# Kernel tuning notes

Measured on AMD Instinct MI355X. Metric: run time of the kernel, lower is better.

Reference implementation:

```python
import jax, jax.numpy as jnp
import numpy as np

N_POI, EMBED, N_EDGES, N_LAYERS, N_HEADS = 50000, 128, 800000, 2, 4
B, L = 512, 64  # sessions, session length (equal-length sections)


def setup_inputs() -> dict:
    key = jax.random.key(0)
    ks = jax.random.split(key, 12)
    d = EMBED
    return {
        "poi_embeds": jax.random.normal(ks[0], (N_POI, d), jnp.float32),
        "dist_edges": jax.random.randint(ks[1], (2, N_EDGES), 0, N_POI),
        "dist_vec": jax.random.uniform(ks[2], (N_EDGES,), jnp.float32),
        "data_poi": jax.random.randint(ks[3], (B,), 0, N_POI),
        "data_x": jax.random.randint(ks[4], (B * L,), 0, N_POI),
        "lin_w": jax.random.normal(ks[5], (N_LAYERS, d, d), jnp.float32) / np.sqrt(d),
        "lin_b": jnp.zeros((N_LAYERS, d), jnp.float32),
        "in_proj_w": jax.random.normal(ks[6], (3 * d, d), jnp.float32) / np.sqrt(d),
        "in_proj_b": jnp.zeros((3 * d,), jnp.float32),
        "out_proj_w": jax.random.normal(ks[7], (d, d), jnp.float32) / np.sqrt(d),
        "out_proj_b": jnp.zeros((d,), jnp.float32),
    }


def reference(poi_embeds, dist_edges, dist_vec, data_poi, data_x,
              lin_w, lin_b, in_proj_w, in_proj_b, out_proj_w, out_proj_b):
    n_poi, d = poi_embeds.shape
    # --- edge augmentation done in GeoGraph.__init__: reversed edges + self loops ---
    loop = jnp.arange(n_poi)
    edges = jnp.concatenate([dist_edges, dist_edges[::-1], jnp.stack([loop, loop])], axis=1)
    dvec = jnp.concatenate([dist_vec, dist_vec, jnp.zeros((n_poi,), dist_vec.dtype)])
    src, dst = edges[0], edges[1]
    # degree of source nodes (torch_geometric.utils.degree on nodes1)
    deg = jnp.zeros((n_poi,), poi_embeds.dtype).at[src].add(1.0)
    w = jax.lax.rsqrt(deg[src] * deg[dst]) * jnp.exp(-dvec ** 2)  # [E]

    enc = poi_embeds
    for i in range(lin_w.shape[0]):
        h = enc @ lin_w[i].T + lin_b[i]                              # [N, d]
        msg = w[:, None] * h[dst]                                    # [E, d] gather
        agg = jax.ops.segment_sum(msg, src, num_segments=n_poi)      # [N, d] scatter
        agg = jnp.where(agg >= 0, agg, 0.01 * agg)                   # leaky_relu(0.01)
        enc = agg / jnp.maximum(jnp.linalg.norm(agg, axis=-1, keepdims=True), 1e-12)

    tar_embed = enc[data_poi]                                        # [B, d]
    seq = enc[data_x].reshape(B, L, d)                               # padded sessions

    # --- nn.MultiheadAttention (batch_first) ---
    hd = d // N_HEADS
    qkv = seq @ in_proj_w.T + in_proj_b                              # [B, L, 3d]
    q, k, v = jnp.split(qkv, 3, axis=-1)
    heads = lambda t: t.reshape(B, L, N_HEADS, hd).transpose(0, 2, 1, 3)
    q, k, v = heads(q), heads(k), heads(v)
    scores = jnp.einsum('bhqd,bhkd->bhqk', q, k) / np.sqrt(hd)
    attn = jax.nn.softmax(scores, axis=-1)
    o = jnp.einsum('bhqk,bhkd->bhqd', attn, v).transpose(0, 2, 1, 3).reshape(B, L, d)
    o = o @ out_proj_w.T + out_proj_b

    aggr_feat = o.mean(axis=1)                                       # mean over padded length
    return aggr_feat, tar_embed
```

## Files before the change

kernel.cpp:

```cpp
#include <hip/hip_runtime.h>
#include <hip/hip_fp16.h>
#include <type_traits>

#define NPOI 50000
#define EMB 128
#define NEDGE 800000
#define EAUG (2 * NEDGE + NPOI)
#define BATCH 512
#define SEQL 64
#define NHEADS 4
#define HDIM 32
#define SCAN_BLOCKS ((NPOI + 255) / 256)
#define NB SCAN_BLOCKS
#define P1_BLOCKS ((NEDGE + 2047) / 2048)
#define SLAB_CAP 10240
#define BUCKET_CAP 10240

typedef _Float16 half8 __attribute__((ext_vector_type(8)));
typedef _Float16 half4 __attribute__((ext_vector_type(4)));
typedef _Float16 half2t __attribute__((ext_vector_type(2)));
typedef float f32x4 __attribute__((ext_vector_type(4)));
typedef unsigned long long u64;

union HBits { _Float16 h; unsigned short u; };


#define N4_POI (NPOI * 128 / 4)
#define N4_LIN (2 * 128 * 128 / 4)
#define N4_INW (384 * 128 / 4)

__global__ void cvt_all_kernel(const float* __restrict__ poi, const float* __restrict__ linw,
                               const float* __restrict__ inw,
                               _Float16* __restrict__ poi_h, _Float16* __restrict__ linw_h,
                               _Float16* __restrict__ inw_h) {
    int i = blockIdx.x * blockDim.x + threadIdx.x;
    const float* src; _Float16* dst; int j = i;
    if (i < N4_POI) { src = poi; dst = poi_h; }
    else if (i < N4_POI + N4_LIN) { j = i - N4_POI; src = linw; dst = linw_h; }
    else if (i < N4_POI + N4_LIN + N4_INW) { j = i - N4_POI - N4_LIN; src = inw; dst = inw_h; }
    else return;
    float4 v = ((const float4*)src)[j];
    half4 h = { (_Float16)v.x, (_Float16)v.y, (_Float16)v.z, (_Float16)v.w };
    ((half4*)dst)[j] = h;
}

__global__ void init_bcur_kernel(int* __restrict__ bcur) {
    int t = blockIdx.x * blockDim.x + threadIdx.x;
    if (t < NB) bcur[t] = t * SLAB_CAP;
}


__global__ __launch_bounds__(256) void partition_kernel(
    const int* __restrict__ e0, const int* __restrict__ e1,
    const float* __restrict__ dv, int* __restrict__ bcur,
    u64* __restrict__ staging)
{
    __shared__ u64 stg[4096];
    __shared__ int lh[NB], lbase[NB], gb[NB];
    __shared__ int sc[256];
    const int t = threadIdx.x;
    const int blockBase = blockIdx.x * 2048;
    for (int j = t; j < NB; j += 256) lh[j] = 0;
    __syncthreads();

    u64 vals[16];
    unsigned br[16];
#pragma unroll
    for (int i = 0; i < 8; ++i) {
        br[2 * i] = 0xFFFFFFFFu;
        br[2 * i + 1] = 0xFFFFFFFFu;
        int g = blockBase + i * 256 + t;
        if (g < NEDGE) {
            int s = e0[g], d = e1[g];
            unsigned db = __float_as_uint(dv[g]);
            vals[2 * i]     = ((u64)s << 48) | ((u64)d << 32) | db;
            vals[2 * i + 1] = ((u64)d << 48) | ((u64)s << 32) | db;
            int bs = s >> 8, bd = d >> 8;
            int rs = atomicAdd(&lh[bs], 1);
            int rd_ = atomicAdd(&lh[bd], 1);
            br[2 * i]     = ((unsigned)bs << 16) | (unsigned)rs;
            br[2 * i + 1] = ((unsigned)bd << 16) | (unsigned)rd_;
        }
    }
    __syncthreads();
    sc[t] = (t < NB) ? lh[t] : 0;
    __syncthreads();
    for (int o = 1; o < 256; o <<= 1) {
        int u = (t >= o) ? sc[t - o] : 0;
        __syncthreads();
        sc[t] += u;
        __syncthreads();
    }
    if (t < NB) {
        lbase[t] = sc[t] - lh[t];
        gb[t] = (lh[t] > 0) ? atomicAdd(&bcur[t], lh[t]) : 0;
    }
    __syncthreads();
#pragma unroll
    for (int i = 0; i < 16; ++i) {
        if (br[i] != 0xFFFFFFFFu) {
            int b = br[i] >> 16, r = br[i] & 0xFFFF;
            stg[lbase[b] + r] = vals[i];
        }
    }
    __syncthreads();
    const int total = sc[255];
    for (int j = t; j < total; j += 256) {
        u64 v = stg[j];
        int b = (int)(v >> 56);
        staging[(size_t)gb[b] + (unsigned)(j - lbase[b])] = v;
    }
}


__global__ __launch_bounds__(256) void hist_kernel(const u64* __restrict__ staging,
                                                   const int* __restrict__ bcur,
                                                   int* __restrict__ counts,
                                                   int* __restrict__ bsum) {
    __shared__ int cnt[256];
    __shared__ int red[256];
    const int b = blockIdx.x, t = threadIdx.x;
    cnt[t] = 0;
    __syncthreads();
    const int base = b * SLAB_CAP;
    const int n = bcur[b] - base;
    for (int j = t; j < n; j += 256)
        atomicAdd(&cnt[(int)(staging[base + j] >> 48) & 255], 1);
    __syncthreads();
    int node = b * 256 + t;
    int rowsz = 0;
    if (node < NPOI) {
        counts[node] = cnt[t];
        rowsz = cnt[t] + 1;
    }
    red[t] = rowsz;
    __syncthreads();
    for (int o = 128; o > 0; o >>= 1) {
        if (t < o) red[t] += red[t + o];
        __syncthreads();
    }
    if (t == 0) bsum[b] = red[0];
}

__global__ __launch_bounds__(256) void scan_chunk_kernel(const int* __restrict__ counts,
                                                         const int* __restrict__ bsum,
                                                         int* __restrict__ offs,
                                                         float* __restrict__ rd) {
    __shared__ int shb[256];
    __shared__ int sh[256];
    __shared__ int base_sh;
    int b = blockIdx.x, t = threadIdx.x;
    shb[t] = (t < SCAN_BLOCKS) ? bsum[t] : 0;
    __syncthreads();
    int partial = 0;
    for (int j = t; j < b; j += 256) partial += shb[j];
    sh[t] = partial;
    __syncthreads();
    for (int o = 128; o > 0; o >>= 1) {
        if (t < o) sh[t] += sh[t + o];
        __syncthreads();
    }
    if (t == 0) base_sh = sh[0];
    __syncthreads();
    int bbase = base_sh;
    __syncthreads();
    int i = b * 256 + t;
    int v = (i < NPOI) ? (counts[i] + 1) : 0;
    sh[t] = v;
    __syncthreads();
    for (int o = 1; o < 256; o <<= 1) {
        int u = (t >= o) ? sh[t - o] : 0;
        __syncthreads();
        sh[t] += u;
        __syncthreads();
    }
    int excl = sh[t] - v + bbase;
    if (i < NPOI) {
        offs[i] = excl;
        rd[i] = rsqrtf((float)v);
        if (i == NPOI - 1) offs[NPOI] = excl + v;
    }
}


__global__ __launch_bounds__(256) void csr_sort_kernel(
    const u64* __restrict__ staging, const int* __restrict__ bcur,
    const int* __restrict__ offs, const float* __restrict__ rd,
    unsigned* __restrict__ ew)
{
    const int k = blockIdx.x;
    const int node0 = k * 256;
    const int node1 = (node0 + 256 < NPOI) ? node0 + 256 : NPOI;
    __shared__ unsigned outb[BUCKET_CAP];
    __shared__ int cnt[256], base2[256];
    __shared__ float rdl[256];
    const int t = threadIdx.x;
    const int node = node0 + t;
    cnt[t] = 0;
    rdl[t] = (node < NPOI) ? rd[node] : 0.f;
    __syncthreads();
    const int sb = k * SLAB_CAP;
    const int n = bcur[k] - sb;
    for (int j = t; j < n; j += 256)
        atomicAdd(&cnt[(int)(staging[sb + j] >> 48) & 255], 1);
    __syncthreads();
    int rowsz = (node < NPOI) ? cnt[t] + 1 : 0;
    base2[t] = rowsz;
    __syncthreads();
    for (int o = 1; o < 256; o <<= 1) {
        int u = (t >= o) ? base2[t - o] : 0;
        __syncthreads();
        base2[t] += u;
        __syncthreads();
    }
    int myexc = base2[t] - rowsz;
    __syncthreads();
    base2[t] = myexc;
    cnt[t] = 0;
    __syncthreads();
    for (int j = t; j < n; j += 256) {
        u64 e = staging[sb + j];
        int sl = (int)(e >> 48) & 255;
        int d = (int)(e >> 32) & 0xFFFF;
        float dist = __uint_as_float((unsigned)e);
        float w = rdl[sl] * rd[d] * expf(-dist * dist);
        HBits cv; cv.h = (_Float16)w;
        int r = atomicAdd(&cnt[sl], 1);
        outb[base2[sl] + r] = ((unsigned)d << 16) | cv.u;
    }
    __syncthreads();
    if (node < NPOI) {
        float w = rdl[t] * rdl[t];
        HBits cv; cv.h = (_Float16)w;
        outb[base2[t] + cnt[t]] = ((unsigned)node << 16) | cv.u;
    }
    __syncthreads();
    const int beg = offs[node0];
    const int ntot = offs[node1] - beg;
    for (int j = t; j < ntot; j += 256) ew[beg + j] = outb[j];
}


template <typename OutT>
__global__ __launch_bounds__(256) void gemm_mfma_f16(
    const _Float16* __restrict__ A, const int* __restrict__ gidx,
    const _Float16* __restrict__ B, const float* __restrict__ bias,
    OutT* __restrict__ C, int M, int N)
{
    __shared__ _Float16 Asl[64][136];
    __shared__ _Float16 Bsl[64][136];
    const int tid = threadIdx.x;
    const int n0 = blockIdx.x * 64;
    const int m0 = blockIdx.y * 64;

#pragma unroll
    for (int i = 0; i < 4; ++i) {
        int u = i * 256 + tid;
        int r = u >> 4;
        int c = u & 15;
        int row = m0 + r;
        int ar = (row < M) ? (gidx ? gidx[row] : row) : 0;
        *(float4*)&Asl[r][c * 8] = *(const float4*)(A + (size_t)ar * 128 + c * 8);
        *(float4*)&Bsl[r][c * 8] = *(const float4*)(B + (size_t)(n0 + r) * 128 + c * 8);
    }
    __syncthreads();

    const int wave = tid >> 6;
    const int lane = tid & 63;
    const int l15 = lane & 15;
    const int quad = lane >> 4;

    f32x4 acc[4];
#pragma unroll
    for (int mt = 0; mt < 4; ++mt) acc[mt] = (f32x4){0.f, 0.f, 0.f, 0.f};

#pragma unroll
    for (int ks = 0; ks < 4; ++ks) {
        half8 bfrag = *(const half8*)&Bsl[wave * 16 + l15][quad * 8 + ks * 32];
#pragma unroll
        for (int mt = 0; mt < 4; ++mt) {
            half8 afrag = *(const half8*)&Asl[mt * 16 + l15][quad * 8 + ks * 32];
            acc[mt] = __builtin_amdgcn_mfma_f32_16x16x32_f16(afrag, bfrag, acc[mt], 0, 0, 0);
        }
    }

    int col = n0 + wave * 16 + l15;
    float bv = bias[col];
#pragma unroll
    for (int mt = 0; mt < 4; ++mt) {
#pragma unroll
        for (int r = 0; r < 4; ++r) {
            int m = m0 + mt * 16 + quad * 4 + r;
            if (m < M) {
                float v = acc[mt][r] + bv;
                if constexpr (std::is_same<OutT, _Float16>::value)
                    C[(size_t)m * N + col] = (_Float16)v;
                else
                    C[(size_t)m * N + col] = v;
            }
        }
    }
}


__global__ __launch_bounds__(64) void aggregate_kernel(
    const _Float16* __restrict__ h, const int* __restrict__ offs,
    const unsigned* __restrict__ ew, float* __restrict__ enc_out,
    _Float16* __restrict__ enc_h)
{
    const int row = blockIdx.x;
    const int lane = threadIdx.x;
    const int beg = offs[row];
    const int end = offs[row + 1];
    float ax = 0.f, ay = 0.f;
#pragma unroll 4
    for (int e = beg; e < end; ++e) {
        unsigned p = ew[e];
        HBits cv; cv.u = (unsigned short)(p & 0xffffu);
        float w = (float)cv.h;
        int d = p >> 16;
        half2t hv = *(const half2t*)(h + (size_t)d * 128 + lane * 2);
        ax += w * (float)hv[0];
        ay += w * (float)hv[1];
    }
    ax = ax >= 0.f ? ax : 0.01f * ax;
    ay = ay >= 0.f ? ay : 0.01f * ay;
    float ss = ax * ax + ay * ay;
#pragma unroll
    for (int o = 32; o > 0; o >>= 1) ss += __shfl_xor(ss, o);
    float inv = 1.f / fmaxf(sqrtf(ss), 1e-12f);
    float ex = ax * inv, ey = ay * inv;
    *(float2*)(enc_out + (size_t)row * 128 + lane * 2) = make_float2(ex, ey);
    half2t hv = { (_Float16)ex, (_Float16)ey };
    *(half2t*)(enc_h + (size_t)row * 128 + lane * 2) = hv;
}


__global__ __launch_bounds__(256) void attn_mfma_kernel(
    const _Float16* __restrict__ qkv, const float* __restrict__ outw,
    const float* __restrict__ outb, float* __restrict__ out)
{
    const int b = blockIdx.x;
    const int wave = threadIdx.x >> 6;
    const int lane = threadIdx.x & 63;
    const int l15 = lane & 15;
    const int quad = lane >> 4;
    __shared__ _Float16 pP[NHEADS][64][72];
    __shared__ _Float16 vT[NHEADS][32][72];
    __shared__ float ob[128];
    const _Float16* base = qkv + (size_t)b * SEQL * 384;

    {
        const _Float16* vrow = base + (size_t)lane * 384 + 256 + wave * 32;
        half8 v0 = *(const half8*)(vrow);
        half8 v1 = *(const half8*)(vrow + 8);
        half8 v2 = *(const half8*)(vrow + 16);
        half8 v3 = *(const half8*)(vrow + 24);
#pragma unroll
        for (int j = 0; j < 8; ++j) {
            vT[wave][j][lane]      = v0[j];
            vT[wave][j + 8][lane]  = v1[j];
            vT[wave][j + 16][lane] = v2[j];
            vT[wave][j + 24][lane] = v3[j];
        }
    }

    half8 qf[4], kf[4];
#pragma unroll
    for (int t = 0; t < 4; ++t) {
        qf[t] = *(const half8*)(base + (size_t)(t * 16 + l15) * 384 + wave * 32 + quad * 8);
        kf[t] = *(const half8*)(base + (size_t)(t * 16 + l15) * 384 + 128 + wave * 32 + quad * 8);
    }

    f32x4 S[4][4];
#pragma unroll
    for (int lt = 0; lt < 4; ++lt)
#pragma unroll
        for (int mt = 0; mt < 4; ++mt) S[lt][mt] = (f32x4){0.f, 0.f, 0.f, 0.f};
#pragma unroll
    for (int lt = 0; lt < 4; ++lt)
#pragma unroll
        for (int mt = 0; mt < 4; ++mt)
            S[lt][mt] = __builtin_amdgcn_mfma_f32_16x16x32_f16(qf[lt], kf[mt], S[lt][mt], 0, 0, 0);

    const float scale = 0.17677669529663687f;
#pragma unroll
    for (int lt = 0; lt < 4; ++lt) {
#pragma unroll
        for (int r = 0; r < 4; ++r) {
            float m0 = -1e30f;
#pragma unroll
            for (int mt = 0; mt < 4; ++mt) {
                S[lt][mt][r] *= scale;
                m0 = fmaxf(m0, S[lt][mt][r]);
            }
#pragma unroll
            for (int o = 1; o < 16; o <<= 1) m0 = fmaxf(m0, __shfl_xor(m0, o));
            float s0 = 0.f;
#pragma unroll
            for (int mt = 0; mt < 4; ++mt) {
                float p = __expf(S[lt][mt][r] - m0);
                S[lt][mt][r] = p;
                s0 += p;
            }
#pragma unroll
            for (int o = 1; o < 16; o <<= 1) s0 += __shfl_xor(s0, o);
            float inv = 1.f / s0;
#pragma unroll
            for (int mt = 0; mt < 4; ++mt)
                pP[wave][lt * 16 + quad * 4 + r][mt * 16 + l15] = (_Float16)(S[lt][mt][r] * inv);
        }
    }
    __syncthreads();

    f32x4 O[4][2];
#pragma unroll
    for (int lt = 0; lt < 4; ++lt)
#pragma unroll
        for (int jt = 0; jt < 2; ++jt) O[lt][jt] = (f32x4){0.f, 0.f, 0.f, 0.f};
#pragma unroll
    for (int kh = 0; kh < 2; ++kh) {
        half8 vf[2];
#pragma unroll
        for (int jt = 0; jt < 2; ++jt)
            vf[jt] = *(const half8*)&vT[wave][jt * 16 + l15][kh * 32 + quad * 8];
#pragma unroll
        for (int lt = 0; lt < 4; ++lt) {
            half8 pf = *(const half8*)&pP[wave][lt * 16 + l15][kh * 32 + quad * 8];
#pragma unroll
            for (int jt = 0; jt < 2; ++jt)
                O[lt][jt] = __builtin_amdgcn_mfma_f32_16x16x32_f16(pf, vf[jt], O[lt][jt], 0, 0, 0);
        }
    }

#pragma unroll
    for (int jt = 0; jt < 2; ++jt) {
        float part = 0.f;
#pragma unroll
        for (int lt = 0; lt < 4; ++lt)
#pragma unroll
            for (int r = 0; r < 4; ++r) part += O[lt][jt][r];
        part += __shfl_xor(part, 16);
        part += __shfl_xor(part, 32);
        if (quad == 0) ob[wave * 32 + jt * 16 + l15] = part * (1.f / 64.f);
    }
    __syncthreads();

    int t = threadIdx.x;
    if (t < 128) {
        float val = outb[t];
        const float* wrow = outw + (size_t)t * 128;
#pragma unroll 8
        for (int k4 = 0; k4 < 32; ++k4) {
            float4 wv = *(const float4*)(wrow + k4 * 4);
            val += wv.x * ob[k4 * 4] + wv.y * ob[k4 * 4 + 1]
                 + wv.z * ob[k4 * 4 + 2] + wv.w * ob[k4 * 4 + 3];
        }
        out[(size_t)b * 128 + t] = val;
    }
}


__global__ void tar_kernel(const float* __restrict__ enc, const int* __restrict__ data_poi,
                           float* __restrict__ out)
{
    int i = blockIdx.x * blockDim.x + threadIdx.x;
    if (i >= BATCH * 128) return;
    int r = i >> 7, c = i & 127;
    out[i] = enc[(size_t)data_poi[r] * 128 + c];
}


extern "C" void kernel_launch(void* const* d_in, const int* in_sizes, int n_in,
                              void* d_out, int out_size, void* d_ws, size_t ws_size,
                              hipStream_t stream)
{
    const float* poi      = (const float*)d_in[0];
    const int*   edges    = (const int*)d_in[1];
    const float* dvec     = (const float*)d_in[2];
    const int*   data_poi = (const int*)d_in[3];
    const int*   data_x   = (const int*)d_in[4];
    const float* lin_w    = (const float*)d_in[5];
    const float* lin_b    = (const float*)d_in[6];
    const float* inw      = (const float*)d_in[7];
    const float* inb      = (const float*)d_in[8];
    const float* outw     = (const float*)d_in[9];
    const float* outb     = (const float*)d_in[10];
    const int* e0 = edges;
    const int* e1 = edges + NEDGE;

    char* ws = (char*)d_ws;
    size_t off = 0;
    auto alloc = [&](size_t bytes) -> void* {
        void* p = ws + off;
        off = (off + bytes + 255) & ~(size_t)255;
        return p;
    };
    int*      counts = (int*)     alloc(NPOI * 4);
    int*      offs   = (int*)     alloc((NPOI + 1) * 4);
    int*      bsum   = (int*)     alloc(SCAN_BLOCKS * 4);
    int*      bcur   = (int*)     alloc(NB * 4);
    float*    rd     = (float*)   alloc(NPOI * 4);
    unsigned* ew     = (unsigned*)alloc((size_t)EAUG * 4);
    float*    enc    = (float*)   alloc((size_t)NPOI * 128 * 4);
    _Float16* enc_h  = (_Float16*)alloc((size_t)NPOI * 128 * 2);
    _Float16* linw_h = (_Float16*)alloc((size_t)2 * 128 * 128 * 2);
    _Float16* inw_h  = (_Float16*)alloc((size_t)384 * 128 * 2);
    char*     big    = (char*)    alloc(50ull * 1024 * 1024);
    _Float16* poi_h   = (_Float16*)big;
    u64*      staging = (u64*)(big + 16ull * 1024 * 1024);
    _Float16* hbuf    = (_Float16*)(big + 33ull * 1024 * 1024);
    _Float16* qkv_h   = (_Float16*)big;

    cvt_all_kernel<<<(N4_POI + N4_LIN + N4_INW + 255) / 256, 256, 0, stream>>>(
        poi, lin_w, inw, poi_h, linw_h, inw_h);

    init_bcur_kernel<<<1, 256, 0, stream>>>(bcur);
    partition_kernel<<<P1_BLOCKS, 256, 0, stream>>>(e0, e1, dvec, bcur, staging);
    hist_kernel<<<NB, 256, 0, stream>>>(staging, bcur, counts, bsum);
    scan_chunk_kernel<<<SCAN_BLOCKS, 256, 0, stream>>>(counts, bsum, offs, rd);
    csr_sort_kernel<<<NB, 256, 0, stream>>>(staging, bcur, offs, rd, ew);

    gemm_mfma_f16<_Float16><<<dim3(2, (NPOI + 63) / 64), 256, 0, stream>>>(
        poi_h, nullptr, linw_h, lin_b, hbuf, NPOI, 128);
    aggregate_kernel<<<NPOI, 64, 0, stream>>>(hbuf, offs, ew, enc, enc_h);
    gemm_mfma_f16<_Float16><<<dim3(2, (NPOI + 63) / 64), 256, 0, stream>>>(
        enc_h, nullptr, linw_h + 128 * 128, lin_b + 128, hbuf, NPOI, 128);
    aggregate_kernel<<<NPOI, 64, 0, stream>>>(hbuf, offs, ew, enc, enc_h);

    gemm_mfma_f16<_Float16><<<dim3(6, BATCH * SEQL / 64), 256, 0, stream>>>(
        enc_h, data_x, inw_h, inb, qkv_h, BATCH * SEQL, 384);
    attn_mfma_kernel<<<BATCH, 256, 0, stream>>>(qkv_h, outw, outb, (float*)d_out);

    tar_kernel<<<(BATCH * 128 + 255) / 256, 256, 0, stream>>>(
        enc, data_poi, (float*)d_out + BATCH * 128);
}
```

Measured before the change: 307.2 us.

## Fuse small setup kernels, stage GEMM epilogue through LDS, merge target gather into attention

```diff
diff --git a/kernel.cpp b/kernel.cpp
--- a/kernel.cpp
+++ b/kernel.cpp
@@ -1,6 +1,5 @@
 #include <hip/hip_runtime.h>
 #include <hip/hip_fp16.h>
-#include <type_traits>
 
 #define NPOI 50000
 #define EMB 128
@@ -10,8 +9,7 @@
 #define SEQL 64
 #define NHEADS 4
 #define HDIM 32
-#define SCAN_BLOCKS ((NPOI + 255) / 256)
-#define NB SCAN_BLOCKS
+#define NB 196
 #define P1_BLOCKS ((NEDGE + 2047) / 2048)
 #define SLAB_CAP 10240
 #define BUCKET_CAP 10240
@@ -28,25 +26,22 @@
 #define N4_POI (NPOI * 128 / 4)
 #define N4_LIN (2 * 128 * 128 / 4)
 #define N4_INW (384 * 128 / 4)
+#define CVT_TOT (N4_POI + N4_LIN + N4_INW + NB)
 
 __global__ void cvt_all_kernel(const float* __restrict__ poi, const float* __restrict__ linw,
                                const float* __restrict__ inw,
                                _Float16* __restrict__ poi_h, _Float16* __restrict__ linw_h,
-                               _Float16* __restrict__ inw_h) {
+                               _Float16* __restrict__ inw_h, int* __restrict__ bcur) {
     int i = blockIdx.x * blockDim.x + threadIdx.x;
     const float* src; _Float16* dst; int j = i;
     if (i < N4_POI) { src = poi; dst = poi_h; }
     else if (i < N4_POI + N4_LIN) { j = i - N4_POI; src = linw; dst = linw_h; }
     else if (i < N4_POI + N4_LIN + N4_INW) { j = i - N4_POI - N4_LIN; src = inw; dst = inw_h; }
+    else if (i < CVT_TOT) { int b = i - (N4_POI + N4_LIN + N4_INW); bcur[b] = b * SLAB_CAP; return; }
     else return;
     float4 v = ((const float4*)src)[j];
     half4 h = { (_Float16)v.x, (_Float16)v.y, (_Float16)v.z, (_Float16)v.w };
     ((half4*)dst)[j] = h;
-}
-
-__global__ void init_bcur_kernel(int* __restrict__ bcur) {
-    int t = blockIdx.x * blockDim.x + threadIdx.x;
-    if (t < NB) bcur[t] = t * SLAB_CAP;
 }
 
 
@@ -115,7 +110,7 @@
 
 __global__ __launch_bounds__(256) void hist_kernel(const u64* __restrict__ staging,
                                                    const int* __restrict__ bcur,
-                                                   int* __restrict__ counts,
+                                                   float* __restrict__ rd,
                                                    int* __restrict__ bsum) {
     __shared__ int cnt[256];
     __shared__ int red[256];
@@ -130,8 +125,8 @@
     int node = b * 256 + t;
     int rowsz = 0;
     if (node < NPOI) {
-        counts[node] = cnt[t];
         rowsz = cnt[t] + 1;
+        rd[node] = rsqrtf((float)rowsz);
     }
     red[t] = rowsz;
     __syncthreads();
@@ -142,62 +137,35 @@
     if (t == 0) bsum[b] = red[0];
 }
 
-__global__ __launch_bounds__(256) void scan_chunk_kernel(const int* __restrict__ counts,
-                                                         const int* __restrict__ bsum,
-                                                         int* __restrict__ offs,
-                                                         float* __restrict__ rd) {
-    __shared__ int shb[256];
-    __shared__ int sh[256];
-    __shared__ int base_sh;
-    int b = blockIdx.x, t = threadIdx.x;
-    shb[t] = (t < SCAN_BLOCKS) ? bsum[t] : 0;
-    __syncthreads();
-    int partial = 0;
-    for (int j = t; j < b; j += 256) partial += shb[j];
-    sh[t] = partial;
-    __syncthreads();
-    for (int o = 128; o > 0; o >>= 1) {
-        if (t < o) sh[t] += sh[t + o];
-        __syncthreads();
-    }
-    if (t == 0) base_sh = sh[0];
-    __syncthreads();
-    int bbase = base_sh;
-    __syncthreads();
-    int i = b * 256 + t;
-    int v = (i < NPOI) ? (counts[i] + 1) : 0;
-    sh[t] = v;
-    __syncthreads();
-    for (int o = 1; o < 256; o <<= 1) {
-        int u = (t >= o) ? sh[t - o] : 0;
-        __syncthreads();
-        sh[t] += u;
-        __syncthreads();
-    }
-    int excl = sh[t] - v + bbase;
-    if (i < NPOI) {
-        offs[i] = excl;
-        rd[i] = rsqrtf((float)v);
-        if (i == NPOI - 1) offs[NPOI] = excl + v;
-    }
-}
-
 
 __global__ __launch_bounds__(256) void csr_sort_kernel(
     const u64* __restrict__ staging, const int* __restrict__ bcur,
-    const int* __restrict__ offs, const float* __restrict__ rd,
-    unsigned* __restrict__ ew)
+    const int* __restrict__ bsum, const float* __restrict__ rd,
+    int* __restrict__ offs, unsigned* __restrict__ ew)
 {
     const int k = blockIdx.x;
     const int node0 = k * 256;
-    const int node1 = (node0 + 256 < NPOI) ? node0 + 256 : NPOI;
     __shared__ unsigned outb[BUCKET_CAP];
     __shared__ int cnt[256], base2[256];
     __shared__ float rdl[256];
+    __shared__ int bb_sh;
     const int t = threadIdx.x;
     const int node = node0 + t;
     cnt[t] = 0;
     rdl[t] = (node < NPOI) ? rd[node] : 0.f;
+    {
+        int partial = 0;
+        for (int j = t; j < k; j += 256) partial += bsum[j];
+        base2[t] = partial;
+        __syncthreads();
+        for (int o = 128; o > 0; o >>= 1) {
+            if (t < o) base2[t] += base2[t + o];
+            __syncthreads();
+        }
+        if (t == 0) bb_sh = base2[0];
+        __syncthreads();
+    }
+    const int bucketbase = bb_sh;
     __syncthreads();
     const int sb = k * SLAB_CAP;
     const int n = bcur[k] - sb;
@@ -217,6 +185,10 @@
     __syncthreads();
     base2[t] = myexc;
     cnt[t] = 0;
+    if (node < NPOI) {
+        offs[node] = bucketbase + myexc;
+        if (node == NPOI - 1) offs[NPOI] = bucketbase + myexc + rowsz;
+    }
     __syncthreads();
     for (int j = t; j < n; j += 256) {
         u64 e = staging[sb + j];
@@ -235,17 +207,15 @@
         outb[base2[t] + cnt[t]] = ((unsigned)node << 16) | cv.u;
     }
     __syncthreads();
-    const int beg = offs[node0];
-    const int ntot = offs[node1] - beg;
-    for (int j = t; j < ntot; j += 256) ew[beg + j] = outb[j];
-}
-
-
-template <typename OutT>
+    const int ntot = (node0 + 256 < NPOI ? n + 256 : n + (NPOI - node0));
+    for (int j = t; j < ntot; j += 256) ew[bucketbase + j] = outb[j];
+}
+
+
 __global__ __launch_bounds__(256) void gemm_mfma_f16(
     const _Float16* __restrict__ A, const int* __restrict__ gidx,
     const _Float16* __restrict__ B, const float* __restrict__ bias,
-    OutT* __restrict__ C, int M, int N)
+    _Float16* __restrict__ C, int M, int N)
 {
     __shared__ _Float16 Asl[64][136];
     __shared__ _Float16 Bsl[64][136];
@@ -284,21 +254,23 @@
         }
     }
 
-    int col = n0 + wave * 16 + l15;
-    float bv = bias[col];
-#pragma unroll
-    for (int mt = 0; mt < 4; ++mt) {
-#pragma unroll
-        for (int r = 0; r < 4; ++r) {
-            int m = m0 + mt * 16 + quad * 4 + r;
-            if (m < M) {
-                float v = acc[mt][r] + bv;
-                if constexpr (std::is_same<OutT, _Float16>::value)
-                    C[(size_t)m * N + col] = (_Float16)v;
-                else
-                    C[(size_t)m * N + col] = v;
-            }
-        }
+    const int col = wave * 16 + l15;
+    const float bv = bias[n0 + col];
+    __syncthreads();
+#pragma unroll
+    for (int mt = 0; mt < 4; ++mt)
+#pragma unroll
+        for (int r = 0; r < 4; ++r)
+            Asl[mt * 16 + quad * 4 + r][col] = (_Float16)(acc[mt][r] + bv);
+    __syncthreads();
+#pragma unroll
+    for (int i = 0; i < 2; ++i) {
+        int u = i * 256 + tid;
+        int r = u >> 3;
+        int c = u & 7;
+        int m = m0 + r;
+        if (m < M)
+            *(half8*)(C + (size_t)m * N + n0 + c * 8) = *(const half8*)&Asl[r][c * 8];
     }
 }
 
@@ -313,7 +285,7 @@
     const int beg = offs[row];
     const int end = offs[row + 1];
     float ax = 0.f, ay = 0.f;
-#pragma unroll 4
+#pragma unroll 8
     for (int e = beg; e < end; ++e) {
         unsigned p = ew[e];
         HBits cv; cv.u = (unsigned short)(p & 0xffffu);
@@ -338,7 +310,8 @@
 
 __global__ __launch_bounds__(256) void attn_mfma_kernel(
     const _Float16* __restrict__ qkv, const float* __restrict__ outw,
-    const float* __restrict__ outb, float* __restrict__ out)
+    const float* __restrict__ outb, const float* __restrict__ enc,
+    const int* __restrict__ data_poi, float* __restrict__ out)
 {
     const int b = blockIdx.x;
     const int wave = threadIdx.x >> 6;
@@ -457,17 +430,10 @@
                  + wv.z * ob[k4 * 4 + 2] + wv.w * ob[k4 * 4 + 3];
         }
         out[(size_t)b * 128 + t] = val;
-    }
-}
-
-
-__global__ void tar_kernel(const float* __restrict__ enc, const int* __restrict__ data_poi,
-                           float* __restrict__ out)
-{
-    int i = blockIdx.x * blockDim.x + threadIdx.x;
-    if (i >= BATCH * 128) return;
-    int r = i >> 7, c = i & 127;
-    out[i] = enc[(size_t)data_poi[r] * 128 + c];
+    } else {
+        int j = t - 128;
+        out[(size_t)(BATCH + b) * 128 + j] = enc[(size_t)data_poi[b] * 128 + j];
+    }
 }
 
 
@@ -496,9 +462,8 @@
         off = (off + bytes + 255) & ~(size_t)255;
         return p;
     };
-    int*      counts = (int*)     alloc(NPOI * 4);
     int*      offs   = (int*)     alloc((NPOI + 1) * 4);
-    int*      bsum   = (int*)     alloc(SCAN_BLOCKS * 4);
+    int*      bsum   = (int*)     alloc(NB * 4);
     int*      bcur   = (int*)     alloc(NB * 4);
     float*    rd     = (float*)   alloc(NPOI * 4);
     unsigned* ew     = (unsigned*)alloc((size_t)EAUG * 4);
@@ -512,26 +477,21 @@
     _Float16* hbuf    = (_Float16*)(big + 33ull * 1024 * 1024);
     _Float16* qkv_h   = (_Float16*)big;
 
-    cvt_all_kernel<<<(N4_POI + N4_LIN + N4_INW + 255) / 256, 256, 0, stream>>>(
-        poi, lin_w, inw, poi_h, linw_h, inw_h);
-
-    init_bcur_kernel<<<1, 256, 0, stream>>>(bcur);
+    cvt_all_kernel<<<(CVT_TOT + 255) / 256, 256, 0, stream>>>(
+        poi, lin_w, inw, poi_h, linw_h, inw_h, bcur);
+
     partition_kernel<<<P1_BLOCKS, 256, 0, stream>>>(e0, e1, dvec, bcur, staging);
-    hist_kernel<<<NB, 256, 0, stream>>>(staging, bcur, counts, bsum);
-    scan_chunk_kernel<<<SCAN_BLOCKS, 256, 0, stream>>>(counts, bsum, offs, rd);
-    csr_sort_kernel<<<NB, 256, 0, stream>>>(staging, bcur, offs, rd, ew);
-
-    gemm_mfma_f16<_Float16><<<dim3(2, (NPOI + 63) / 64), 256, 0, stream>>>(
+    hist_kernel<<<NB, 256, 0, stream>>>(staging, bcur, rd, bsum);
+    csr_sort_kernel<<<NB, 256, 0, stream>>>(staging, bcur, bsum, rd, offs, ew);
+
+    gemm_mfma_f16<<<dim3(2, (NPOI + 63) / 64), 256, 0, stream>>>(
         poi_h, nullptr, linw_h, lin_b, hbuf, NPOI, 128);
     aggregate_kernel<<<NPOI, 64, 0, stream>>>(hbuf, offs, ew, enc, enc_h);
-    gemm_mfma_f16<_Float16><<<dim3(2, (NPOI + 63) / 64), 256, 0, stream>>>(
+    gemm_mfma_f16<<<dim3(2, (NPOI + 63) / 64), 256, 0, stream>>>(
         enc_h, nullptr, linw_h + 128 * 128, lin_b + 128, hbuf, NPOI, 128);
     aggregate_kernel<<<NPOI, 64, 0, stream>>>(hbuf, offs, ew, enc, enc_h);
 
-    gemm_mfma_f16<_Float16><<<dim3(6, BATCH * SEQL / 64), 256, 0, stream>>>(
+    gemm_mfma_f16<<<dim3(6, BATCH * SEQL / 64), 256, 0, stream>>>(
         enc_h, data_x, inw_h, inb, qkv_h, BATCH * SEQL, 384);
-    attn_mfma_kernel<<<BATCH, 256, 0, stream>>>(qkv_h, outw, outb, (float*)d_out);
-
-    tar_kernel<<<(BATCH * 128 + 255) / 256, 256, 0, stream>>>(
-        enc, data_poi, (float*)d_out + BATCH * 128);
-}
+    attn_mfma_kernel<<<BATCH, 256, 0, stream>>>(qkv_h, outw, outb, enc, data_poi, (float*)d_out);
+}
```

Measured after the change: 288.5 us. 6.1% less time.
